# Performance work log

Hardware: AMD Instinct MI355X
Metric: run time of the kernel (lower is better)

Reference implementation:

```python
import jax, jax.numpy as jnp
import numpy as np

N_EMBD = 768
N_HEAD = 12
HEAD_DIM = N_EMBD // N_HEAD
LN_EPS = 1e-5


def setup_inputs() -> dict:
    key = jax.random.key(0)
    ks = jax.random.split(key, 12)
    s = 0.02
    B, T = 8, 1024
    return {
        "x": jax.random.normal(ks[0], (B, T, N_EMBD), dtype=jnp.float32),
        "ln1_g": jnp.ones((N_EMBD,), jnp.float32),
        "ln1_b": jnp.zeros((N_EMBD,), jnp.float32),
        "w_attn": jax.random.normal(ks[1], (N_EMBD, 3 * N_EMBD), jnp.float32) * s,
        "b_attn": jnp.zeros((3 * N_EMBD,), jnp.float32),
        "w_proj": jax.random.normal(ks[2], (N_EMBD, N_EMBD), jnp.float32) * s,
        "b_proj": jnp.zeros((N_EMBD,), jnp.float32),
        "ln2_g": jnp.ones((N_EMBD,), jnp.float32),
        "ln2_b": jnp.zeros((N_EMBD,), jnp.float32),
        "w_fc1": jax.random.normal(ks[3], (N_EMBD, 4 * N_EMBD), jnp.float32) * s,
        "b_fc1": jnp.zeros((4 * N_EMBD,), jnp.float32),
        "w_fc2": jax.random.normal(ks[4], (4 * N_EMBD, N_EMBD), jnp.float32) * s,
        "b_fc2": jnp.zeros((N_EMBD,), jnp.float32),
    }


def _layernorm(x, g, b):
    mu = jnp.mean(x, axis=-1, keepdims=True)
    var = jnp.mean(jnp.square(x - mu), axis=-1, keepdims=True)
    return (x - mu) * jax.lax.rsqrt(var + LN_EPS) * g + b


def _block(x, ln1_g, ln1_b, w_attn, b_attn, w_proj, b_proj,
           ln2_g, ln2_b, w_fc1, b_fc1, w_fc2, b_fc2):
    B, T, C = x.shape
    # --- causal self-attention (dropout inactive in eval) ---
    h = _layernorm(x, ln1_g, ln1_b)
    qkv = h @ w_attn + b_attn                      # [B,T,3C]
    q, k, v = jnp.split(qkv, 3, axis=-1)
    q = q.reshape(B, T, N_HEAD, HEAD_DIM).transpose(0, 2, 1, 3)  # [B,H,T,D]
    k = k.reshape(B, T, N_HEAD, HEAD_DIM).transpose(0, 2, 1, 3)
    v = v.reshape(B, T, N_HEAD, HEAD_DIM).transpose(0, 2, 1, 3)
    att = jnp.einsum('bhtd,bhsd->bhts', q, k) * (1.0 / np.sqrt(HEAD_DIM))
    mask = jnp.tril(jnp.ones((T, T), dtype=bool))
    att = jnp.where(mask, att, -jnp.inf)
    att = jax.nn.softmax(att, axis=-1)
    y = jnp.einsum('bhts,bhsd->bhtd', att, v)
    y = y.transpose(0, 2, 1, 3).reshape(B, T, C)
    x = x + y @ w_proj + b_proj
    # --- MLP ---
    h2 = _layernorm(x, ln2_g, ln2_b)
    h2 = jax.nn.gelu(h2 @ w_fc1 + b_fc1, approximate=True)
    x = x + h2 @ w_fc2 + b_fc2
    return x


def reference(x, ln1_g, ln1_b, w_attn, b_attn, w_proj, b_proj,
              ln2_g, ln2_b, w_fc1, b_fc1, w_fc2, b_fc2):
    return _block(x, ln1_g, ln1_b, w_attn, b_attn, w_proj, b_proj,
                  ln2_g, ln2_b, w_fc1, b_fc1, w_fc2, b_fc2)
```

## Files before the change

### kernel.cpp

```cpp
#include <hip/hip_runtime.h>
#include <cstdint>
#include <cmath>

typedef unsigned short u16;
typedef __bf16 bf16_t;
typedef bf16_t bf16x8 __attribute__((ext_vector_type(8)));
typedef float f32x4 __attribute__((ext_vector_type(4)));
typedef u16 u16x8 __attribute__((ext_vector_type(8)));
typedef u16 u16x4 __attribute__((ext_vector_type(4)));

#define DEV __device__ __forceinline__

DEV u16 f2b(float f) {
    uint32_t u = __builtin_bit_cast(uint32_t, f);
    u += 0x7FFFu + ((u >> 16) & 1u);
    return (u16)(u >> 16);
}
DEV float b2f(u16 h) { return __builtin_bit_cast(float, (uint32_t)h << 16); }

DEV bf16x8 load8(const u16* p) {
    return __builtin_bit_cast(bf16x8, *reinterpret_cast<const u16x8*>(p));
}

DEV void async16(void* lds, const void* g) {
    __builtin_amdgcn_global_load_lds(
        reinterpret_cast<const __attribute__((address_space(1))) void*>(
            reinterpret_cast<uintptr_t>(g)),
        reinterpret_cast<__attribute__((address_space(3))) void*>(
            reinterpret_cast<uintptr_t>(lds)),
        16, 0, 0);
}

DEV float gelu_t(float x) {
    float z = 0.7978845608028654f * (x + 0.044715f * x * x * x);
    z = fminf(fmaxf(z, -15.0f), 15.0f);
    float e = __expf(2.0f * z);
    return 0.5f * x * (1.0f + (e - 1.0f) / (e + 1.0f));
}

__global__ __launch_bounds__(256) void ln_k(const float* __restrict__ x,
                                            const float* __restrict__ g,
                                            const float* __restrict__ bb,
                                            u16* __restrict__ out) {
    const int lane = threadIdx.x & 63, w = threadIdx.x >> 6;
    const int row = blockIdx.x * 4 + w;
    const float4* xr = reinterpret_cast<const float4*>(x + (size_t)row * 768);
    float4 v[3];
    float s = 0.f, s2 = 0.f;
#pragma unroll
    for (int i = 0; i < 3; ++i) {
        v[i] = xr[i * 64 + lane];
        s += v[i].x + v[i].y + v[i].z + v[i].w;
        s2 += v[i].x * v[i].x + v[i].y * v[i].y + v[i].z * v[i].z + v[i].w * v[i].w;
    }
#pragma unroll
    for (int off = 1; off < 64; off <<= 1) {
        s += __shfl_xor(s, off);
        s2 += __shfl_xor(s2, off);
    }
    const float mu = s * (1.0f / 768.0f);
    const float rstd = rsqrtf(s2 * (1.0f / 768.0f) - mu * mu + 1e-5f);
#pragma unroll
    for (int i = 0; i < 3; ++i) {
        int col = i * 256 + lane * 4;
        u16x4 o;
        o[0] = f2b((v[i].x - mu) * rstd * g[col + 0] + bb[col + 0]);
        o[1] = f2b((v[i].y - mu) * rstd * g[col + 1] + bb[col + 1]);
        o[2] = f2b((v[i].z - mu) * rstd * g[col + 2] + bb[col + 2]);
        o[3] = f2b((v[i].w - mu) * rstd * g[col + 3] + bb[col + 3]);
        *reinterpret_cast<u16x4*>(out + (size_t)row * 768 + col) = o;
    }
}

__global__ __launch_bounds__(256) void wconv_k(const float* __restrict__ W,
                                               u16* __restrict__ WT, int K, int N) {
    __shared__ float tile[32][33];
    const int tx = threadIdx.x, ty = threadIdx.y;
    const int n0 = blockIdx.x * 32, k0 = blockIdx.y * 32;
#pragma unroll
    for (int i = 0; i < 4; ++i)
        tile[ty + i * 8][tx] = W[(size_t)(k0 + ty + i * 8) * N + n0 + tx];
    __syncthreads();
#pragma unroll
    for (int i = 0; i < 4; ++i)
        WT[(size_t)(n0 + ty + i * 8) * K + k0 + tx] = f2b(tile[tx][ty + i * 8]);
}

__global__ __launch_bounds__(256) void vtrans_k(const u16* __restrict__ qkv,
                                                u16* __restrict__ vT) {
    __shared__ u16 tile[32][33];
    const int tx = threadIdx.x, ty = threadIdx.y;
    const int t0 = blockIdx.x * 32, d0 = blockIdx.y * 32, bh = blockIdx.z;
    const int b = bh / 12, hd = bh % 12;
#pragma unroll
    for (int i = 0; i < 4; ++i)
        tile[ty + i * 8][tx] =
            qkv[(size_t)(b * 1024 + t0 + ty + i * 8) * 2304 + 1536 + hd * 64 + d0 + tx];
    __syncthreads();
#pragma unroll
    for (int i = 0; i < 4; ++i)
        vT[(size_t)(bh * 64 + d0 + ty + i * 8) * 1024 + t0 + tx] = tile[tx][ty + i * 8];
}

template <int ACT, int RESID, int OUTBF>
__global__ __launch_bounds__(256) void gemm_bt(const u16* __restrict__ A,
                                               const u16* __restrict__ BT,
                                               const float* __restrict__ bias,
                                               const float* __restrict__ resid,
                                               void* __restrict__ out,
                                               int M, int N, int K) {
    __shared__ u16 As[3][128 * 32];
    __shared__ u16 Bs[3][128 * 32];
    const int tid = threadIdx.x, lane = tid & 63;
    const int l15 = lane & 15, lg = lane >> 4;
    const int nx = gridDim.x;
    const int bid = blockIdx.y * nx + blockIdx.x;
    const int q = (nx * gridDim.y) >> 3;
    const int swz = (bid & 7) * q + (bid >> 3);
    const int mBase = (swz / nx) * 128, nBase = (swz % nx) * 128;
    const int w = tid >> 6, wr = w >> 1, wc = w & 1;

    auto stage = [&](int buf, int kk) {
        const int k0 = kk << 5;
#pragma unroll
        for (int i = 0; i < 2; ++i) {
            int c = i * 256 + tid;
            int row = c >> 2, colE = (c & 3) << 3;
            async16(As[buf] + c * 8, A + (size_t)(mBase + row) * K + k0 + colE);
        }
#pragma unroll
        for (int i = 0; i < 2; ++i) {
            int c = i * 256 + tid;
            int row = c >> 2, colE = (c & 3) << 3;
            async16(Bs[buf] + c * 8, BT + (size_t)(nBase + row) * K + k0 + colE);
        }
    };

    f32x4 acc[4][4] = {};
    const int nsteps = K >> 5;
    stage(0, 0);
    stage(1, 1);
    int cur = 0;
    for (int kk = 0; kk < nsteps; ++kk) {
        if (kk + 2 < nsteps) {
            int nb = cur + 2;
            if (nb >= 3) nb -= 3;
            stage(nb, kk + 2);
            asm volatile("s_waitcnt vmcnt(8)" ::: "memory");
        } else if (kk + 1 < nsteps) {
            asm volatile("s_waitcnt vmcnt(4)" ::: "memory");
        } else {
            asm volatile("s_waitcnt vmcnt(0)" ::: "memory");
        }
        __builtin_amdgcn_s_barrier();
        asm volatile("" ::: "memory");

        bf16x8 af[4], bfr[4];
#pragma unroll
        for (int mi = 0; mi < 4; ++mi)
            af[mi] = load8(As[cur] + (wr * 64 + mi * 16 + l15) * 32 + lg * 8);
#pragma unroll
        for (int ni = 0; ni < 4; ++ni)
            bfr[ni] = load8(Bs[cur] + (wc * 64 + ni * 16 + l15) * 32 + lg * 8);
        __builtin_amdgcn_s_setprio(1);
#pragma unroll
        for (int mi = 0; mi < 4; ++mi)
#pragma unroll
            for (int ni = 0; ni < 4; ++ni)
                acc[mi][ni] = __builtin_amdgcn_mfma_f32_16x16x32_bf16(
                    af[mi], bfr[ni], acc[mi][ni], 0, 0, 0);
        __builtin_amdgcn_s_setprio(0);

        asm volatile("" ::: "memory");
        __builtin_amdgcn_s_barrier();
        cur = (cur == 2) ? 0 : cur + 1;
    }
#pragma unroll
    for (int mi = 0; mi < 4; ++mi) {
#pragma unroll
        for (int ni = 0; ni < 4; ++ni) {
            const int row0 = mBase + wr * 64 + mi * 16 + lg * 4;
            const int col = nBase + wc * 64 + ni * 16 + l15;
            const float bv = bias[col];
#pragma unroll
            for (int r = 0; r < 4; ++r) {
                float v = acc[mi][ni][r] + bv;
                if (ACT == 1) v = gelu_t(v);
                size_t off = (size_t)(row0 + r) * N + col;
                if (RESID) v += resid[off];
                if (OUTBF)
                    ((u16*)out)[off] = f2b(v);
                else
                    ((float*)out)[off] = v;
            }
        }
    }
}

__global__ __launch_bounds__(256, 3) void attn_k(const u16* __restrict__ qkv,
                                                 const u16* __restrict__ vT,
                                                 u16* __restrict__ y) {
    __shared__ u16 Ks[2][64 * 64];
    __shared__ u16 Vs[2][64 * 64];
    __shared__ u16 Ps[4][2][16 * 64];
    const int tid = threadIdx.x, lane = tid & 63, w = tid >> 6;
    const int bid = blockIdx.x;
    const uint32_t permPk = 2u | (7u << 3) | (1u << 6) | (4u << 9) | (6u << 12) |
                            (0u << 15) | (5u << 18) | (3u << 21);
    const int qt = (permPk >> (((bid + (bid >> 8)) & 7) * 3)) & 7;
    const int bh = ((bid >> 8) << 5) + ((bid & 255) >> 3);
    const int b = bh / 12, hd = bh % 12;
    const int l15 = lane & 15, lg = lane >> 4;
    const int r0 = qt * 128 + w * 32;

    const float qscale = 0.125f * 1.4426950408889634f;
    bf16x8 qf[2][2];
#pragma unroll
    for (int m = 0; m < 2; ++m) {
        const u16* qb = qkv + (size_t)(b * 1024 + r0 + m * 16 + l15) * 2304 + hd * 64;
#pragma unroll
        for (int ks = 0; ks < 2; ++ks) {
            u16x8 u = *reinterpret_cast<const u16x8*>(qb + ks * 32 + lg * 8);
            u16x8 o;
#pragma unroll
            for (int jj = 0; jj < 8; ++jj) o[jj] = f2b(b2f(u[jj]) * qscale);
            qf[m][ks] = __builtin_bit_cast(bf16x8, o);
        }
    }

    const u16* kbase = qkv + (size_t)(b * 1024) * 2304 + 768 + hd * 64;
    const u16* vbase = vT + (size_t)(bh * 64) * 1024;

    auto stage = [&](int buf, int j) {
#pragma unroll
        for (int i = 0; i < 2; ++i) {
            int c = i * 256 + tid;
            int row = c >> 3, sc = ((c & 7) ^ (row & 7)) << 3;
            async16(Ks[buf] + c * 8, kbase + (size_t)(j * 64 + row) * 2304 + sc);
        }
#pragma unroll
        for (int i = 0; i < 2; ++i) {
            int c = i * 256 + tid;
            int row = c >> 3, sc = ((c & 7) ^ (row & 7)) << 3;
            async16(Vs[buf] + c * 8, vbase + (size_t)row * 1024 + j * 64 + sc);
        }
    };

    f32x4 oacc[2][4] = {};
    float mrow[2] = {-1e30f, -1e30f};
    float lrow[2] = {0.f, 0.f};

    const int jd = (r0 + 31) >> 6;
    const int jmax = qt * 2 + 1;

    stage(0, 0);
    for (int j = 0; j <= jmax; ++j) {
        const int cur = j & 1;
        if (j < jmax) {
            stage(cur ^ 1, j + 1);
            asm volatile("s_waitcnt vmcnt(4)" ::: "memory");
        } else {
            asm volatile("s_waitcnt vmcnt(0)" ::: "memory");
        }
        __builtin_amdgcn_s_barrier();
        asm volatile("" ::: "memory");

        if (j <= jd) {
            const bool diag = (j == jd);
            const u16* Kc = Ks[cur];
            const u16* Vc = Vs[cur];
            f32x4 s[2][4] = {};
            __builtin_amdgcn_s_setprio(1);
#pragma unroll
            for (int ks = 0; ks < 2; ++ks) {
                bf16x8 kf[4];
#pragma unroll
                for (int ni = 0; ni < 4; ++ni) {
                    int key = ni * 16 + l15;
                    kf[ni] = load8(Kc + key * 64 + (((ks * 4 + lg) ^ (key & 7)) << 3));
                }
#pragma unroll
                for (int ni = 0; ni < 4; ++ni) {
                    s[0][ni] = __builtin_amdgcn_mfma_f32_16x16x32_bf16(
                        kf[ni], qf[0][ks], s[0][ni], 0, 0, 0);
                    s[1][ni] = __builtin_amdgcn_mfma_f32_16x16x32_bf16(
                        kf[ni], qf[1][ks], s[1][ni], 0, 0, 0);
                }
            }
            __builtin_amdgcn_s_setprio(0);

#pragma unroll
            for (int m = 0; m < 2; ++m) {
                if (diag) {
                    const int qrow = r0 + m * 16 + l15;
#pragma unroll
                    for (int ni = 0; ni < 4; ++ni) {
                        int key = j * 64 + ni * 16 + lg * 4;
#pragma unroll
                        for (int r = 0; r < 4; ++r)
                            if (key + r > qrow) s[m][ni][r] = -1e30f;
                    }
                }
                float pmax = -1e30f;
#pragma unroll
                for (int ni = 0; ni < 4; ++ni)
#pragma unroll
                    for (int r = 0; r < 4; ++r) pmax = fmaxf(pmax, s[m][ni][r]);
                pmax = fmaxf(pmax, __shfl_xor(pmax, 16));
                pmax = fmaxf(pmax, __shfl_xor(pmax, 32));

                if (!__all(pmax <= mrow[m] + 8.0f)) {
                    float mnew = fmaxf(mrow[m], pmax);
                    float scal = exp2f(mrow[m] - mnew);
                    mrow[m] = mnew;
                    lrow[m] *= scal;
#pragma unroll
                    for (int r = 0; r < 4; ++r) {
                        float sr = __shfl(scal, lg * 4 + r);
#pragma unroll
                        for (int ni = 0; ni < 4; ++ni) oacc[m][ni][r] *= sr;
                    }
                }
                float psum = 0.f;
#pragma unroll
                for (int ni = 0; ni < 4; ++ni) {
                    u16x4 pk;
#pragma unroll
                    for (int r = 0; r < 4; ++r) {
                        float pv = exp2f(s[m][ni][r] - mrow[m]);
                        psum += pv;
                        pk[r] = f2b(pv);
                    }
                    *reinterpret_cast<u16x4*>(
                        &Ps[w][m][l15 * 64 + ((ni * 16 + lg * 4) ^ ((l15 & 7) << 3))]) =
                        pk;
                }
                psum += __shfl_xor(psum, 16);
                psum += __shfl_xor(psum, 32);
                lrow[m] += psum;
            }

            __builtin_amdgcn_s_setprio(1);
#pragma unroll
            for (int ks = 0; ks < 2; ++ks) {
                bf16x8 pf0 = load8(
                    &Ps[w][0][l15 * 64 + ((ks * 32 + lg * 8) ^ ((l15 & 7) << 3))]);
                bf16x8 pf1 = load8(
                    &Ps[w][1][l15 * 64 + ((ks * 32 + lg * 8) ^ ((l15 & 7) << 3))]);
                bf16x8 vf[4];
#pragma unroll
                for (int ni = 0; ni < 4; ++ni) {
                    int d = ni * 16 + l15;
                    vf[ni] = load8(Vc + d * 64 + (((ks * 4 + lg) ^ (d & 7)) << 3));
                }
#pragma unroll
                for (int ni = 0; ni < 4; ++ni) {
                    oacc[0][ni] = __builtin_amdgcn_mfma_f32_16x16x32_bf16(
                        pf0, vf[ni], oacc[0][ni], 0, 0, 0);
                    oacc[1][ni] = __builtin_amdgcn_mfma_f32_16x16x32_bf16(
                        pf1, vf[ni], oacc[1][ni], 0, 0, 0);
                }
            }
            __builtin_amdgcn_s_setprio(0);
        }
        asm volatile("" ::: "memory");
        __builtin_amdgcn_s_barrier();
        asm volatile("" ::: "memory");
    }

#pragma unroll
    for (int m = 0; m < 2; ++m) {
#pragma unroll
        for (int r = 0; r < 4; ++r) {
            float rl = 1.0f / __shfl(lrow[m], lg * 4 + r);
            int row = r0 + m * 16 + lg * 4 + r;
#pragma unroll
            for (int ni = 0; ni < 4; ++ni) {
                int col = hd * 64 + ni * 16 + l15;
                y[(size_t)(b * 1024 + row) * 768 + col] = f2b(oacc[m][ni][r] * rl);
            }
        }
    }
}

extern "C" void kernel_launch(void* const* d_in, const int* in_sizes, int n_in,
                              void* d_out, int out_size, void* d_ws, size_t ws_size,
                              hipStream_t stream) {
    const float* x      = (const float*)d_in[0];
    const float* ln1_g  = (const float*)d_in[1];
    const float* ln1_b  = (const float*)d_in[2];
    const float* w_attn = (const float*)d_in[3];
    const float* b_attn = (const float*)d_in[4];
    const float* w_proj = (const float*)d_in[5];
    const float* b_proj = (const float*)d_in[6];
    const float* ln2_g  = (const float*)d_in[7];
    const float* ln2_b  = (const float*)d_in[8];
    const float* w_fc1  = (const float*)d_in[9];
    const float* b_fc1  = (const float*)d_in[10];
    const float* w_fc2  = (const float*)d_in[11];
    const float* b_fc2  = (const float*)d_in[12];
    float* out = (float*)d_out;

    char* p = (char*)d_ws;
    auto take = [&](size_t n) {
        char* r = p;
        p += (n + 255) & ~(size_t)255;
        return r;
    };
    u16* wT_attn = (u16*)take((size_t)2304 * 768 * 2);
    u16* wT_proj = (u16*)take((size_t)768 * 768 * 2);
    u16* wT_fc1  = (u16*)take((size_t)3072 * 768 * 2);
    u16* wT_fc2  = (u16*)take((size_t)768 * 3072 * 2);
    u16* h       = (u16*)take((size_t)8192 * 768 * 2);
    u16* bufA    = (u16*)take((size_t)50331648);
    u16* yb      = (u16*)take((size_t)8192 * 768 * 2);
    float* x1    = (float*)take((size_t)8192 * 768 * 4);
    u16* qkv = bufA;
    u16* vT  = bufA + (size_t)8192 * 2304;
    u16* g1  = bufA;

    const dim3 tb(32, 8);
    wconv_k<<<dim3(2304 / 32, 768 / 32), tb, 0, stream>>>(w_attn, wT_attn, 768, 2304);
    wconv_k<<<dim3(768 / 32, 768 / 32), tb, 0, stream>>>(w_proj, wT_proj, 768, 768);
    wconv_k<<<dim3(3072 / 32, 768 / 32), tb, 0, stream>>>(w_fc1, wT_fc1, 768, 3072);
    wconv_k<<<dim3(768 / 32, 3072 / 32), tb, 0, stream>>>(w_fc2, wT_fc2, 3072, 768);
    ln_k<<<2048, 256, 0, stream>>>(x, ln1_g, ln1_b, h);
    gemm_bt<0, 0, 1><<<dim3(18, 64), 256, 0, stream>>>(h, wT_attn, b_attn, nullptr,
                                                       qkv, 8192, 2304, 768);
    vtrans_k<<<dim3(32, 2, 96), tb, 0, stream>>>(qkv, vT);
    attn_k<<<768, 256, 0, stream>>>(qkv, vT, yb);
    gemm_bt<0, 1, 0><<<dim3(6, 64), 256, 0, stream>>>(yb, wT_proj, b_proj, x,
                                                      x1, 8192, 768, 768);
    ln_k<<<2048, 256, 0, stream>>>(x1, ln2_g, ln2_b, h);
    gemm_bt<1, 0, 1><<<dim3(24, 64), 256, 0, stream>>>(h, wT_fc1, b_fc1, nullptr,
                                                       g1, 8192, 3072, 768);
    gemm_bt<0, 1, 0><<<dim3(6, 64), 256, 0, stream>>>(g1, wT_fc2, b_fc2, x1,
                                                      out, 8192, 768, 3072);
}
```

Measured before the change: 260.4 us.

## Swizzle GEMM LDS tiles, use double buffering, and store residual x1 as bf16

```diff
diff --git a/kernel.cpp b/kernel.cpp
--- a/kernel.cpp
+++ b/kernel.cpp
@@ -72,6 +72,44 @@
     }
 }
 
+__global__ __launch_bounds__(256) void ln_b16(const u16* __restrict__ x,
+                                              const float* __restrict__ g,
+                                              const float* __restrict__ bb,
+                                              u16* __restrict__ out) {
+    const int lane = threadIdx.x & 63, w = threadIdx.x >> 6;
+    const int row = blockIdx.x * 4 + w;
+    const u16* xr = x + (size_t)row * 768;
+    float v[12];
+    float s = 0.f, s2 = 0.f;
+#pragma unroll
+    for (int i = 0; i < 3; ++i) {
+        u16x4 u = *reinterpret_cast<const u16x4*>(xr + i * 256 + lane * 4);
+#pragma unroll
+        for (int jj = 0; jj < 4; ++jj) {
+            float f = b2f(u[jj]);
+            v[i * 4 + jj] = f;
+            s += f;
+            s2 += f * f;
+        }
+    }
+#pragma unroll
+    for (int off = 1; off < 64; off <<= 1) {
+        s += __shfl_xor(s, off);
+        s2 += __shfl_xor(s2, off);
+    }
+    const float mu = s * (1.0f / 768.0f);
+    const float rstd = rsqrtf(s2 * (1.0f / 768.0f) - mu * mu + 1e-5f);
+#pragma unroll
+    for (int i = 0; i < 3; ++i) {
+        int col = i * 256 + lane * 4;
+        u16x4 o;
+#pragma unroll
+        for (int jj = 0; jj < 4; ++jj)
+            o[jj] = f2b((v[i * 4 + jj] - mu) * rstd * g[col + jj] + bb[col + jj]);
+        *reinterpret_cast<u16x4*>(out + (size_t)row * 768 + col) = o;
+    }
+}
+
 __global__ __launch_bounds__(256) void wconv_k(const float* __restrict__ W,
                                                u16* __restrict__ WT, int K, int N) {
     __shared__ float tile[32][33];
@@ -102,15 +140,15 @@
         vT[(size_t)(bh * 64 + d0 + ty + i * 8) * 1024 + t0 + tx] = tile[tx][ty + i * 8];
 }
 
-template <int ACT, int RESID, int OUTBF>
+template <int ACT, int RESIDT, int OUTBF>
 __global__ __launch_bounds__(256) void gemm_bt(const u16* __restrict__ A,
                                                const u16* __restrict__ BT,
                                                const float* __restrict__ bias,
-                                               const float* __restrict__ resid,
+                                               const void* __restrict__ resid,
                                                void* __restrict__ out,
                                                int M, int N, int K) {
-    __shared__ u16 As[3][128 * 32];
-    __shared__ u16 Bs[3][128 * 32];
+    __shared__ u16 As[2][128 * 32];
+    __shared__ u16 Bs[2][128 * 32];
     const int tid = threadIdx.x, lane = tid & 63;
     const int l15 = lane & 15, lg = lane >> 4;
     const int nx = gridDim.x;
@@ -125,29 +163,26 @@
 #pragma unroll
         for (int i = 0; i < 2; ++i) {
             int c = i * 256 + tid;
-            int row = c >> 2, colE = (c & 3) << 3;
-            async16(As[buf] + c * 8, A + (size_t)(mBase + row) * K + k0 + colE);
+            int row = c >> 2;
+            int g = ((c & 3) ^ ((row >> 1) & 3)) << 3;
+            async16(As[buf] + c * 8, A + (size_t)(mBase + row) * K + k0 + g);
         }
 #pragma unroll
         for (int i = 0; i < 2; ++i) {
             int c = i * 256 + tid;
-            int row = c >> 2, colE = (c & 3) << 3;
-            async16(Bs[buf] + c * 8, BT + (size_t)(nBase + row) * K + k0 + colE);
+            int row = c >> 2;
+            int g = ((c & 3) ^ ((row >> 1) & 3)) << 3;
+            async16(Bs[buf] + c * 8, BT + (size_t)(nBase + row) * K + k0 + g);
         }
     };
 
     f32x4 acc[4][4] = {};
     const int nsteps = K >> 5;
     stage(0, 0);
-    stage(1, 1);
-    int cur = 0;
     for (int kk = 0; kk < nsteps; ++kk) {
-        if (kk + 2 < nsteps) {
-            int nb = cur + 2;
-            if (nb >= 3) nb -= 3;
-            stage(nb, kk + 2);
-            asm volatile("s_waitcnt vmcnt(8)" ::: "memory");
-        } else if (kk + 1 < nsteps) {
+        const int cur = kk & 1;
+        if (kk + 1 < nsteps) {
+            stage(cur ^ 1, kk + 1);
             asm volatile("s_waitcnt vmcnt(4)" ::: "memory");
         } else {
             asm volatile("s_waitcnt vmcnt(0)" ::: "memory");
@@ -157,11 +192,15 @@
 
         bf16x8 af[4], bfr[4];
 #pragma unroll
-        for (int mi = 0; mi < 4; ++mi)
-            af[mi] = load8(As[cur] + (wr * 64 + mi * 16 + l15) * 32 + lg * 8);
-#pragma unroll
-        for (int ni = 0; ni < 4; ++ni)
-            bfr[ni] = load8(Bs[cur] + (wc * 64 + ni * 16 + l15) * 32 + lg * 8);
+        for (int mi = 0; mi < 4; ++mi) {
+            int rA = wr * 64 + mi * 16 + l15;
+            af[mi] = load8(As[cur] + rA * 32 + ((lg ^ ((rA >> 1) & 3)) << 3));
+        }
+#pragma unroll
+        for (int ni = 0; ni < 4; ++ni) {
+            int rB = wc * 64 + ni * 16 + l15;
+            bfr[ni] = load8(Bs[cur] + rB * 32 + ((lg ^ ((rB >> 1) & 3)) << 3));
+        }
         __builtin_amdgcn_s_setprio(1);
 #pragma unroll
         for (int mi = 0; mi < 4; ++mi)
@@ -173,7 +212,7 @@
 
         asm volatile("" ::: "memory");
         __builtin_amdgcn_s_barrier();
-        cur = (cur == 2) ? 0 : cur + 1;
+        asm volatile("" ::: "memory");
     }
 #pragma unroll
     for (int mi = 0; mi < 4; ++mi) {
@@ -187,7 +226,8 @@
                 float v = acc[mi][ni][r] + bv;
                 if (ACT == 1) v = gelu_t(v);
                 size_t off = (size_t)(row0 + r) * N + col;
-                if (RESID) v += resid[off];
+                if (RESIDT == 1) v += ((const float*)resid)[off];
+                if (RESIDT == 2) v += b2f(((const u16*)resid)[off]);
                 if (OUTBF)
                     ((u16*)out)[off] = f2b(v);
                 else
@@ -414,7 +454,7 @@
     u16* h       = (u16*)take((size_t)8192 * 768 * 2);
     u16* bufA    = (u16*)take((size_t)50331648);
     u16* yb      = (u16*)take((size_t)8192 * 768 * 2);
-    float* x1    = (float*)take((size_t)8192 * 768 * 4);
+    u16* x1b     = (u16*)take((size_t)8192 * 768 * 2);
     u16* qkv = bufA;
     u16* vT  = bufA + (size_t)8192 * 2304;
     u16* g1  = bufA;
@@ -429,11 +469,11 @@
                                                        qkv, 8192, 2304, 768);
     vtrans_k<<<dim3(32, 2, 96), tb, 0, stream>>>(qkv, vT);
     attn_k<<<768, 256, 0, stream>>>(qkv, vT, yb);
-    gemm_bt<0, 1, 0><<<dim3(6, 64), 256, 0, stream>>>(yb, wT_proj, b_proj, x,
-                                                      x1, 8192, 768, 768);
-    ln_k<<<2048, 256, 0, stream>>>(x1, ln2_g, ln2_b, h);
+    gemm_bt<0, 1, 1><<<dim3(6, 64), 256, 0, stream>>>(yb, wT_proj, b_proj, x,
+                                                      x1b, 8192, 768, 768);
+    ln_b16<<<2048, 256, 0, stream>>>(x1b, ln2_g, ln2_b, h);
     gemm_bt<1, 0, 1><<<dim3(24, 64), 256, 0, stream>>>(h, wT_fc1, b_fc1, nullptr,
                                                        g1, 8192, 3072, 768);
-    gemm_bt<0, 1, 0><<<dim3(6, 64), 256, 0, stream>>>(g1, wT_fc2, b_fc2, x1,
+    gemm_bt<0, 2, 0><<<dim3(6, 64), 256, 0, stream>>>(g1, wT_fc2, b_fc2, x1b,
                                                       out, 8192, 768, 3072);
 }
```

New measurement: 254.6 us. -2.2%, faster.
